# Kernel tuning notes

Hardware: AMD Instinct MI355X
Metric: run time of the kernel (lower is better)

## Reference

```python
import jax, jax.numpy as jnp
import numpy as np

B, T, N = 16, 1024, 128
WIN, STEP = 30, 2
MOMENT_ORDERS = (2, 4, 8)
D_MODEL = 256


def _mask_diag(corr):
    n = corr.shape[-1]
    eye = jnp.eye(n, dtype=corr.dtype)
    return corr * (1.0 - eye) + eye


def corrcoef_time(xw):
    # xw: [..., L, N] -> corr over channels: [..., N, N]
    L = xw.shape[-2]
    xm = xw - xw.mean(axis=-2, keepdims=True)
    cov = jnp.einsum('...ln,...lm->...nm', xm, xm) / (L - 1 + 1e-8)
    var = jnp.clip(jnp.diagonal(cov, axis1=-2, axis2=-1), 1e-8, None)
    std = jnp.sqrt(var)
    corr = cov / (std[..., :, None] * std[..., None, :])
    corr = jnp.nan_to_num(corr, nan=0.0, posinf=0.0, neginf=0.0)
    return _mask_diag(corr)


def rowwise_corr(M):
    # M: [B, N, F]
    Xc = M - M.mean(axis=-1, keepdims=True)
    num = jnp.einsum('bnf,bmf->bnm', Xc, Xc)
    den1 = jnp.sqrt(jnp.clip((Xc ** 2).sum(axis=-1), 1e-8, None))
    corr = num / (den1[:, :, None] * den1[:, None, :])
    corr = jnp.nan_to_num(corr, nan=0.0, posinf=0.0, neginf=0.0)
    return _mask_diag(corr)


def layer_norm(x, gamma, beta, eps=1e-5):
    mu = x.mean(axis=-1, keepdims=True)
    var = ((x - mu) ** 2).mean(axis=-1, keepdims=True)
    return (x - mu) / jnp.sqrt(var + eps) * gamma + beta


def normalize_adj(adj):
    n = adj.shape[-1]
    A_hat = adj + jnp.eye(n, dtype=adj.dtype)
    d = A_hat.sum(axis=-1)
    dis = jnp.sqrt(1.0 / jnp.clip(d, 1e-8, None))
    return A_hat * dis[:, :, None] * dis[:, None, :]


def setup_inputs() -> dict:
    key = jax.random.key(0)
    ks = jax.random.split(key, 8)
    in_dim = len(MOMENT_ORDERS) * N
    return {
        'x': jax.random.normal(ks[0], (B, T, N), dtype=jnp.float32),
        'ln_gamma': jnp.ones((in_dim,), jnp.float32),
        'ln_beta': jnp.zeros((in_dim,), jnp.float32),
        'W1': jax.random.normal(ks[1], (in_dim, D_MODEL), jnp.float32) * 0.05,
        'b1': jnp.zeros((D_MODEL,), jnp.float32),
        'W2': jax.random.normal(ks[2], (D_MODEL, D_MODEL), jnp.float32) * 0.05,
        'b2': jnp.zeros((D_MODEL,), jnp.float32),
        'Wc': jax.random.normal(ks[3], (D_MODEL, 1), jnp.float32) * 0.05,
        'bc': jnp.zeros((1,), jnp.float32),
    }


def reference(x, ln_gamma, ln_beta, W1, b1, W2, b2, Wc, bc):
    # sliding windows (static indices)
    starts = np.arange(0, T - WIN + 1, STEP)
    idx = starts[:, None] + np.arange(WIN)[None, :]
    xw = x[:, idx, :]
    lo = corrcoef_time(xw)                            # [B, Wn, N, N]

    mean_lo = lo.mean(axis=1, keepdims=True)
    centered = lo - mean_lo
    cm_list, ho_list = [], []
    for d in MOMENT_ORDERS:
        cm = jnp.nan_to_num((centered ** d).mean(axis=1),
                            nan=0.0, posinf=0.0, neginf=0.0)  # [B, N, N]
        cm_list.append(cm)
        ho_list.append(rowwise_corr(cm))

    X = jnp.concatenate(cm_list, axis=-1)             # [B, N, 3N]
    X = layer_norm(X, ln_gamma, ln_beta)

    A = jnp.stack(ho_list, axis=1).mean(axis=1)
    A = 0.5 * (A + jnp.swapaxes(A, 1, 2))
    A_norm = normalize_adj(A)

    H = jax.nn.relu(jnp.einsum('bnm,bmd->bnd', A_norm, X @ W1 + b1))
    H = jax.nn.relu(jnp.einsum('bnm,bmd->bnd', A_norm, H @ W2 + b2))
    g = H.mean(axis=1)                                # [B, d_model]
    out = jax.nn.sigmoid(g @ Wc + bc)                 # [B, 1]
    return out
```

## Files before the change

### kernel.cpp

```cpp
#include <hip/hip_runtime.h>
#include <math.h>

#define BB  16
#define TT  1024
#define NN  128
#define WIN 30
#define NWD 498
#define DM  256
#define IND 384
#define GW  16

#define INV_W (1.0f/498.0f)

#define SARR (BB*NN*NN)

#define OFF_A     0
#define OFF_G     (OFF_A    + BB*NWD*NN)
#define OFF_CM2   (OFF_G    + BB*NWD*NN)
#define OFF_CM4   (OFF_CM2  + SARR)
#define OFF_CM8   (OFF_CM4  + SARR)
#define OFF_AD    (OFF_CM8  + SARR)
#define OFF_PART  (OFF_AD   + 3*SARR)
#define OFF_ANORM OFF_PART
#define OFF_BUFA  (OFF_ANORM + SARR)
#define OFF_BUFB  (OFF_BUFA + BB*NN*DM)
#define OFF_CTR   (OFF_PART + 768*16384)
#define OFF_GW1   OFF_A
#define OFF_SG    (OFF_GW1 + IND*DM)
#define OFF_SB    (OFF_SG  + DM)

#define GLL16(gsrc, ldst) \
    __builtin_amdgcn_global_load_lds((const __attribute__((address_space(1))) void*)(gsrc), \
                                     (__attribute__((address_space(3))) void*)(ldst), 16, 0, 0)

__global__ __launch_bounds__(128) void k1_stats(const float* __restrict__ x, float* __restrict__ ws) {
    int bx = blockIdx.x;
    if (bx == 0 && threadIdx.x < 128) ((unsigned*)(ws + OFF_CTR))[threadIdx.x] = 0u;
    int c = bx & 15, b = bx >> 4;
    int w0 = c*32, w1 = min(NWD, w0+32);
    int n = threadIdx.x;
    const float* xp = x + (size_t)b*TT*NN + n;

    float sum = 0.f, sq = 0.f;
    for (int t = 2*w0; t < 2*w0 + WIN; ++t) {
        float v = xp[(size_t)t*NN];
        sum += v; sq = fmaf(v, v, sq);
    }
    for (int w = w0; w < w1; ++w) {
        if (w > w0) {
            float o0 = xp[(size_t)(2*w-2)*NN], o1 = xp[(size_t)(2*w-1)*NN];
            float n0 = xp[(size_t)(2*w+28)*NN], n1 = xp[(size_t)(2*w+29)*NN];
            sum += (n0 + n1) - (o0 + o1);
            sq  += (n0*n0 + n1*n1) - (o0*o0 + o1*o1);
        }
        float mean = sum * (1.0f/30.0f);
        float ss = sq - 30.0f*mean*mean;
        float var = fmaxf(ss * (1.0f/29.0f), 1e-8f);
        float a = (1.0f / sqrtf(var)) * 0.185695338f;
        ws[OFF_A + ((size_t)b*NWD + w)*NN + n] = a;
        ws[OFF_G + ((size_t)b*NWD + w)*NN + n] = mean * a * 5.477225575f;
    }
}

__global__ __launch_bounds__(256) __attribute__((amdgpu_waves_per_eu(3, 3)))
void k24_inc(const float* __restrict__ x, float* __restrict__ ws) {
    __shared__ __align__(16) float xr[64][NN];
    __shared__ __align__(16) float sa[GW][NN];
    __shared__ __align__(16) float sg[GW][NN];
    int bx = blockIdx.x;
    int wc = bx & 7;
    int slab = (bx >> 3) % 6;
    int b = bx / 48;
    const char IS[6] = {0,0,0,0,1,1};
    const char JS[6] = {0,1,2,3,2,3};
    int is = IS[slab], js = JS[slab];
    int w0 = wc * 63, w1 = min(NWD, w0 + 63);
    int tid = threadIdx.x;
    int jg = tid & 7, ig = tid >> 3;
    int i0 = is*64 + ig*2;
    int j0 = js*32 + jg*4;

    const float* xb = x + (size_t)b*TT*NN;
    const float* Ab = ws + OFF_A + (size_t)b*NWD*NN;
    const float* Gb = ws + OFF_G + (size_t)b*NWD*NN;

    float P[2][4];
    float S1[2][4], S2[2][4], S3[2][4], S4[2][4], S5[2][4], S6[2][4], S7[2][4], S8[2][4];
#pragma unroll
    for (int p=0;p<2;++p)
#pragma unroll
        for (int q=0;q<4;++q) {
            P[p][q]=0.f;
            S1[p][q]=0.f;S2[p][q]=0.f;S3[p][q]=0.f;S4[p][q]=0.f;
            S5[p][q]=0.f;S6[p][q]=0.f;S7[p][q]=0.f;S8[p][q]=0.f;
        }

    auto moments = [&](int k) {
        float2 ai = *(const float2*)&sa[k][i0];
        float2 gi = *(const float2*)&sg[k][i0];
        float4 aj = *(const float4*)&sa[k][j0];
        float4 gj = *(const float4*)&sg[k][j0];
        float av[2] = {ai.x, ai.y};
        float mg[2] = {-gi.x, -gi.y};
        float aw[4] = {aj.x, aj.y, aj.z, aj.w};
        float gw[4] = {gj.x, gj.y, gj.z, gj.w};
#pragma unroll
        for (int p=0;p<2;++p)
#pragma unroll
            for (int q=0;q<4;++q) {
                float aa  = av[p]*aw[q];
                float ngg = mg[p]*gw[q];
                float c   = fmaf(P[p][q], aa, ngg);
                float c2 = c*c;
                float c3 = c2*c;
                float c4 = c2*c2;
                S1[p][q] += c;
                S2[p][q] += c2;
                S3[p][q] += c3;
                S4[p][q] += c4;
                S5[p][q] = fmaf(c4, c,  S5[p][q]);
                S6[p][q] = fmaf(c3, c3, S6[p][q]);
                S7[p][q] = fmaf(c3, c4, S7[p][q]);
                S8[p][q] = fmaf(c4, c4, S8[p][q]);
            }
    };

    int rlo = 2*w0;
    for (int wg = w0; wg < w1; wg += GW) {
        int m = min(GW, w1 - wg);
        __syncthreads();
        int rhi = 2*(wg + m - 1) + 29;
        int nr = rhi - rlo + 1;
        for (int idx = tid; idx < nr*32; idx += 256) {
            int r = idx >> 5, c4 = idx & 31;
            int t = rlo + r;
            GLL16(xb + (size_t)t*NN + c4*4, &xr[t & 63][c4*4]);
        }
        for (int idx = tid; idx < m*32; idx += 256) {
            int k = idx >> 5, c4 = idx & 31;
            GLL16(Ab + (size_t)(wg+k)*NN + c4*4, &sa[k][c4*4]);
        }
        for (int idx = tid; idx < m*32; idx += 256) {
            int k = idx >> 5, c4 = idx & 31;
            GLL16(Gb + (size_t)(wg+k)*NN + c4*4, &sg[k][c4*4]);
        }
        rlo = rhi + 1;
        __syncthreads();

        int kstart = 0;
        if (wg == w0) {
#pragma unroll 6
            for (int k = 0; k < WIN; ++k) {
                int t = 2*w0 + k;
                float2 xi = *(const float2*)&xr[t & 63][i0];
                float4 xj = *(const float4*)&xr[t & 63][j0];
                float av[2] = {xi.x, xi.y};
                float bv[4] = {xj.x, xj.y, xj.z, xj.w};
#pragma unroll
                for (int p=0;p<2;++p)
#pragma unroll
                    for (int q=0;q<4;++q) P[p][q] = fmaf(av[p], bv[q], P[p][q]);
            }
            moments(0);
            kstart = 1;
        }
        for (int k = kstart; k < m; ++k) {
            int w = wg + k;
            int tr[4] = {2*w - 2, 2*w - 1, 2*w + 28, 2*w + 29};
#pragma unroll
            for (int kk = 0; kk < 4; ++kk) {
                int t = tr[kk];
                float sgn = (kk < 2) ? -1.0f : 1.0f;
                float2 xi = *(const float2*)&xr[t & 63][i0];
                float4 xj = *(const float4*)&xr[t & 63][j0];
                float av[2] = {sgn*xi.x, sgn*xi.y};
                float bv[4] = {xj.x, xj.y, xj.z, xj.w};
#pragma unroll
                for (int p=0;p<2;++p)
#pragma unroll
                    for (int q=0;q<4;++q) P[p][q] = fmaf(av[p], bv[q], P[p][q]);
            }
            moments(k);
        }
    }

    float* tp = ws + OFF_PART + (size_t)bx*16384 + tid*8;
#define STORE_ARR(A, S) \
    *(float4*)&tp[(A)*2048]     = make_float4(S[0][0], S[0][1], S[0][2], S[0][3]); \
    *(float4*)&tp[(A)*2048 + 4] = make_float4(S[1][0], S[1][1], S[1][2], S[1][3]);
    STORE_ARR(0, S1) STORE_ARR(1, S2) STORE_ARR(2, S3) STORE_ARR(3, S4)
    STORE_ARR(4, S5) STORE_ARR(5, S6) STORE_ARR(6, S7) STORE_ARR(7, S8)
#undef STORE_ARR
}

__global__ __launch_bounds__(256) void kred(const float* __restrict__ gamma, const float* __restrict__ beta,
                                            const float* __restrict__ W1, float* __restrict__ ws) {
    int bxg = blockIdx.x;
    int tid = threadIdx.x;
    if (bxg >= 768) {
        int gi = bxg - 768;
        if (gi < 96) {
#pragma unroll
            for (int kk = 0; kk < 4; ++kk) {
                int k = gi*4 + kk;
                ws[OFF_GW1 + (size_t)k*DM + tid] = gamma[k] * W1[(size_t)k*DM + tid];
            }
        } else {
            float sgv = 0.f, sbv = 0.f;
            for (int k = 0; k < IND; ++k) {
                float w = W1[(size_t)k*DM + tid];
                sgv = fmaf(gamma[k], w, sgv);
                sbv = fmaf(beta[k],  w, sbv);
            }
            ws[OFF_SG + tid] = sgv;
            ws[OFF_SB + tid] = sbv;
        }
        return;
    }
    int pair = bxg >> 3, sub = bxg & 7;
    int b = pair / 6, slab = pair % 6;
    const char IS[6] = {0,0,0,0,1,1};
    const char JS[6] = {0,1,2,3,2,3};
    int is = IS[slab], js = JS[slab];
    int off = sub*256 + tid;
    const float* base = ws + OFF_PART + (size_t)(b*48 + slab*8)*16384;

    float E[8];
#pragma unroll
    for (int a=0;a<8;++a) E[a] = 0.f;
    for (int c = 0; c < 8; ++c) {
        const float* tp = base + (size_t)c*16384;
#pragma unroll
        for (int a=0;a<8;++a) E[a] += tp[a*2048 + off];
    }

    int tid_old = off >> 3, e = off & 7;
    int ig = tid_old >> 3, jg = tid_old & 7;
    int p = e >> 2, q = e & 3;
    int i = is*64 + ig*2 + p;
    int j = js*32 + jg*4 + q;

    float cm2, cm4, cm8;
    if (i == j) {
        cm2 = 0.f; cm4 = 0.f; cm8 = 0.f;
    } else {
        float e1 = E[0]*INV_W, e2 = E[1]*INV_W, e3 = E[2]*INV_W, e4 = E[3]*INV_W;
        float e5 = E[4]*INV_W, e6 = E[5]*INV_W, e7 = E[6]*INV_W, e8 = E[7]*INV_W;
        float m  = e1;
        float m2 = m*m, m3 = m2*m, m4 = m2*m2, m5 = m4*m, m6 = m3*m3, m8 = m4*m4;
        cm2 = e2 - m2;
        cm4 = e4 - 4.f*m*e3 + 6.f*m2*e2 - 3.f*m4;
        cm8 = e8 - 8.f*m*e7 + 28.f*m2*e6 - 56.f*m3*e5 + 70.f*m4*e4
                 - 56.f*m5*e3 + 28.f*m6*e2 - 7.f*m8;
    }
    float* C2 = ws + OFF_CM2 + (size_t)b*NN*NN;
    float* C4 = ws + OFF_CM4 + (size_t)b*NN*NN;
    float* C8 = ws + OFF_CM8 + (size_t)b*NN*NN;
    C2[i*NN + j] = cm2; C2[j*NN + i] = cm2;
    C4[i*NN + j] = cm4; C4[j*NN + i] = cm4;
    C8[i*NN + j] = cm8; C8[j*NN + i] = cm8;
}

#define XSTR 132
__global__ __launch_bounds__(256) void kB(const float* __restrict__ b1, float* __restrict__ ws) {
    __shared__ __align__(16) float smem[64*XSTR + 2*NN];
    __shared__ unsigned winB;
    int blk = blockIdx.x, tid = threadIdx.x;
    if (blk < 192) {
        int rem = blk % 12;
        int b = blk / 12, di = rem >> 2, jq = rem & 3;
        float* Xct = smem;
        float* Mr  = smem + 64*XSTR;
        float* Ir  = Mr + NN;
        const float* cm = ws + (di==0 ? OFF_CM2 : (di==1 ? OFF_CM4 : OFF_CM8)) + (size_t)b*NN*NN;
        int n0 = (tid >> 4)*8, m0 = jq*32 + (tid & 15)*2;
        float s1 = 0.f, s2 = 0.f;
        float acc0[8], acc1[8];
#pragma unroll
        for (int k=0;k<8;++k) { acc0[k]=0.f; acc1[k]=0.f; }

        for (int h = 0; h < 2; ++h) {
            __syncthreads();
            for (int idx = tid; idx < NN*64; idx += 256) {
                int n = idx >> 6, f0 = idx & 63;
                Xct[f0*XSTR + n] = cm[n*NN + h*64 + f0];
            }
            __syncthreads();
            if (tid < NN) {
                for (int f0 = 0; f0 < 64; ++f0) {
                    float v = Xct[f0*XSTR + tid];
                    s1 += v; s2 = fmaf(v, v, s2);
                }
            }
            for (int f0 = 0; f0 < 64; ++f0) {
                const float* row = &Xct[f0*XSTR];
                float4 a0 = *(const float4*)&row[n0];
                float4 a1 = *(const float4*)&row[n0+4];
                float2 bm = *(const float2*)&row[m0];
                float av[8] = {a0.x,a0.y,a0.z,a0.w,a1.x,a1.y,a1.z,a1.w};
#pragma unroll
                for (int k=0;k<8;++k) {
                    acc0[k] = fmaf(av[k], bm.x, acc0[k]);
                    acc1[k] = fmaf(av[k], bm.y, acc1[k]);
                }
            }
        }
        __syncthreads();
        if (tid < NN) {
            float mean = s1 * (1.0f/NN);
            Mr[tid] = mean;
            Ir[tid] = 1.0f/sqrtf(fmaxf(s2 - (float)NN*mean*mean, 1e-8f));
        }
        __syncthreads();
        float rm0 = Mr[m0], rm1 = Mr[m0+1], im0 = Ir[m0], im1 = Ir[m0+1];
        float* Ad = ws + OFF_AD + (size_t)(b*3 + di)*NN*NN;
#pragma unroll
        for (int k=0;k<8;++k) {
            int gi = n0+k;
            float rn = Mr[gi], inv = Ir[gi];
            float v0 = (acc0[k] - (float)NN*rn*rm0) * inv * im0;
            float v1 = (acc1[k] - (float)NN*rn*rm1) * inv * im1;
            if (gi == m0)   v0 = 1.0f;
            if (gi == m0+1) v1 = 1.0f;
            Ad[gi*NN + m0]     = v0;
            Ad[gi*NN + m0 + 1] = v1;
        }

        __syncthreads();
        if (tid == 0) {
            unsigned* ctr = (unsigned*)(ws + OFF_CTR);
            unsigned old = __hip_atomic_fetch_add(&ctr[96 + b], 1u,
                                                  __ATOMIC_ACQ_REL, __HIP_MEMORY_SCOPE_AGENT);
            winB = (old == 11u) ? 1u : 0u;
        }
        __syncthreads();
        if (winB) {
            float* dis = smem;
            const float* A0 = ws + OFF_AD + (size_t)(b*3 + 0)*NN*NN;
            const float* A1 = ws + OFF_AD + (size_t)(b*3 + 1)*NN*NN;
            const float* A2 = ws + OFF_AD + (size_t)(b*3 + 2)*NN*NN;
            if (tid < NN) {
                float d = 1.0f;
                for (int m = 0; m < NN; ++m) {
                    int o = tid*NN + m;
                    d += (A0[o] + A1[o] + A2[o]) * (1.0f/3.0f);
                }
                dis[tid] = sqrtf(1.0f / fmaxf(d, 1e-8f));
            }
            __syncthreads();
            float* An = ws + OFF_ANORM + (size_t)b*NN*NN;
            for (int idx = tid; idx < NN*NN; idx += 256) {
                int n = idx >> 7, m = idx & 127;
                float s = (A0[idx] + A1[idx] + A2[idx]) * (1.0f/3.0f);
                float v = s + (n==m ? 1.0f : 0.0f);
                An[idx] = v * dis[n] * dis[m];
            }
        }
    } else {
        int r0 = (blk - 192) * 4;
        float* sms = smem;
        float* srs = smem + 4;
        {
            int rloc = tid >> 6, lane = tid & 63;
            int grow = r0 + rloc;
            int b = grow >> 7, n = grow & 127;
            const float* c2 = ws + OFF_CM2 + ((size_t)b*NN + n)*NN;
            const float* c4 = ws + OFF_CM4 + ((size_t)b*NN + n)*NN;
            const float* c8 = ws + OFF_CM8 + ((size_t)b*NN + n)*NN;
            float s1 = 0.f, s2 = 0.f;
            for (int e = lane; e < IND; e += 64) {
                float v = (e < 128) ? c2[e] : (e < 256) ? c4[e-128] : c8[e-256];
                s1 += v; s2 = fmaf(v, v, s2);
            }
#pragma unroll
            for (int o = 32; o > 0; o >>= 1) {
                s1 += __shfl_down(s1, o, 64);
                s2 += __shfl_down(s2, o, 64);
            }
            if (lane == 0) {
                float mean = s1 * (1.0f/IND);
                sms[rloc] = mean;
                srs[rloc] = 1.0f / sqrtf(s2*(1.0f/IND) - mean*mean + 1e-5f);
            }
        }
        __syncthreads();
        float mean[4], rstd[4];
        const float* xrow[4];
#pragma unroll
        for (int r = 0; r < 4; ++r) {
            mean[r] = sms[r]; rstd[r] = srs[r];
        }
        float acc[4] = {0.f, 0.f, 0.f, 0.f};
        const float* GW1p = ws + OFF_GW1;
#pragma unroll
        for (int seg = 0; seg < 3; ++seg) {
            int offc = (seg==0) ? OFF_CM2 : (seg==1) ? OFF_CM4 : OFF_CM8;
#pragma unroll
            for (int r = 0; r < 4; ++r) {
                int grow = r0 + r;
                xrow[r] = ws + offc + ((size_t)(grow >> 7)*NN + (grow & 127))*NN;
            }
            const float* gseg = GW1p + (size_t)(seg*128)*DM + tid;
            for (int k = 0; k < 128; k += 2) {
                float g0 = gseg[(size_t)(k+0)*DM];
                float g1 = gseg[(size_t)(k+1)*DM];
#pragma unroll
                for (int r = 0; r < 4; ++r) {
                    acc[r] = fmaf(xrow[r][k+0], g0, acc[r]);
                    acc[r] = fmaf(xrow[r][k+1], g1, acc[r]);
                }
            }
        }
        float sgv = ws[OFF_SG + tid];
        float sbb = ws[OFF_SB + tid] + b1[tid];
        float* O = ws + OFF_BUFA;
#pragma unroll
        for (int r = 0; r < 4; ++r)
            O[(size_t)(r0+r)*DM + tid] = rstd[r]*(acc[r] - mean[r]*sgv) + sbb;
    }
}

__global__ __launch_bounds__(256) void k98_propgemm(const float* __restrict__ W2, const float* __restrict__ b2,
                                                    const float* __restrict__ An, const float* __restrict__ Zin,
                                                    float* __restrict__ Out) {
    __shared__ float Hs[8][DM];
    int bx = blockIdx.x;
    int b = bx >> 4, n0 = (bx & 15)*8;
    int tid = threadIdx.x;
    const float* A = An + (size_t)b*NN*NN + (size_t)n0*NN;
    const float* Z = Zin + (size_t)b*NN*DM;
    float acc[8] = {0,0,0,0,0,0,0,0};
    for (int m = 0; m < NN; m += 4) {
        float z0 = Z[(size_t)(m+0)*DM + tid];
        float z1 = Z[(size_t)(m+1)*DM + tid];
        float z2 = Z[(size_t)(m+2)*DM + tid];
        float z3 = Z[(size_t)(m+3)*DM + tid];
#pragma unroll
        for (int r = 0; r < 8; ++r) {
            const float* Ar = A + r*NN + m;
            acc[r] = fmaf(Ar[0], z0, acc[r]);
            acc[r] = fmaf(Ar[1], z1, acc[r]);
            acc[r] = fmaf(Ar[2], z2, acc[r]);
            acc[r] = fmaf(Ar[3], z3, acc[r]);
        }
    }
#pragma unroll
    for (int r = 0; r < 8; ++r) Hs[r][tid] = fmaxf(acc[r], 0.0f);
    __syncthreads();
    float acc2[8];
    float bv = b2[tid];
#pragma unroll
    for (int r = 0; r < 8; ++r) acc2[r] = bv;
    for (int k = 0; k < DM; k += 4) {
        float w0 = W2[(size_t)(k+0)*DM + tid];
        float w1 = W2[(size_t)(k+1)*DM + tid];
        float w2 = W2[(size_t)(k+2)*DM + tid];
        float w3 = W2[(size_t)(k+3)*DM + tid];
#pragma unroll
        for (int r = 0; r < 8; ++r) {
            float4 h = *(const float4*)&Hs[r][k];
            acc2[r] = fmaf(h.x, w0, acc2[r]);
            acc2[r] = fmaf(h.y, w1, acc2[r]);
            acc2[r] = fmaf(h.z, w2, acc2[r]);
            acc2[r] = fmaf(h.w, w3, acc2[r]);
        }
    }
    float* O = Out + (size_t)b*NN*DM;
#pragma unroll
    for (int r = 0; r < 8; ++r) O[(size_t)(n0+r)*DM + tid] = acc2[r];
}

__global__ __launch_bounds__(256) void k9_prop(const float* __restrict__ Wc, const float* __restrict__ bc,
                                               const float* __restrict__ An, const float* __restrict__ Zin,
                                               float* __restrict__ Out,
                                               float* __restrict__ ws, float* __restrict__ outp) {
    __shared__ float red[256];
    __shared__ unsigned win9;
    int bx = blockIdx.x;
    int b = bx >> 4, n0 = (bx & 15)*8;
    int tid = threadIdx.x;
    const float* A = An + (size_t)b*NN*NN + (size_t)n0*NN;
    const float* Z = Zin + (size_t)b*NN*DM;
    float acc[8] = {0,0,0,0,0,0,0,0};
    for (int m = 0; m < NN; m += 4) {
        float z0 = Z[(size_t)(m+0)*DM + tid];
        float z1 = Z[(size_t)(m+1)*DM + tid];
        float z2 = Z[(size_t)(m+2)*DM + tid];
        float z3 = Z[(size_t)(m+3)*DM + tid];
#pragma unroll
        for (int r = 0; r < 8; ++r) {
            const float* Ar = A + r*NN + m;
            acc[r] = fmaf(Ar[0], z0, acc[r]);
            acc[r] = fmaf(Ar[1], z1, acc[r]);
            acc[r] = fmaf(Ar[2], z2, acc[r]);
            acc[r] = fmaf(Ar[3], z3, acc[r]);
        }
    }
    float* O = Out + (size_t)b*NN*DM;
#pragma unroll
    for (int r = 0; r < 8; ++r) O[(size_t)(n0+r)*DM + tid] = fmaxf(acc[r], 0.0f);

    __syncthreads();
    if (tid == 0) {
        unsigned* ctr = (unsigned*)(ws + OFF_CTR);
        unsigned old = __hip_atomic_fetch_add(&ctr[112 + b], 1u,
                                              __ATOMIC_ACQ_REL, __HIP_MEMORY_SCOPE_AGENT);
        win9 = (old == 15u) ? 1u : 0u;
    }
    __syncthreads();
    if (win9) {
        const float* H = Out + (size_t)b*NN*DM;
        float s = 0.f;
        for (int n = 0; n < NN; ++n) s += H[(size_t)n*DM + tid];
        red[tid] = s * (1.0f/NN) * Wc[tid];
        __syncthreads();
        for (int o = 128; o > 0; o >>= 1) { if (tid < o) red[tid] += red[tid+o]; __syncthreads(); }
        if (tid == 0) outp[b] = 1.0f/(1.0f + expf(-(red[0] + bc[0])));
    }
}

extern "C" void kernel_launch(void* const* d_in, const int* in_sizes, int n_in,
                              void* d_out, int out_size, void* d_ws, size_t ws_size,
                              hipStream_t stream) {
    (void)in_sizes; (void)n_in; (void)out_size; (void)ws_size;
    const float* x     = (const float*)d_in[0];
    const float* gamma = (const float*)d_in[1];
    const float* beta  = (const float*)d_in[2];
    const float* W1    = (const float*)d_in[3];
    const float* b1    = (const float*)d_in[4];
    const float* W2    = (const float*)d_in[5];
    const float* b2    = (const float*)d_in[6];
    const float* Wc    = (const float*)d_in[7];
    const float* bc    = (const float*)d_in[8];
    float* ws  = (float*)d_ws;
    float* out = (float*)d_out;

    k1_stats    <<<BB*16,    128, 0, stream>>>(x, ws);
    k24_inc     <<<BB*6*8,   256, 0, stream>>>(x, ws);
    kred        <<<768+96+1, 256, 0, stream>>>(gamma, beta, W1, ws);
    kB          <<<704,      256, 0, stream>>>(b1, ws);
    k98_propgemm<<<BB*16,    256, 0, stream>>>(W2, b2, ws + OFF_ANORM, ws + OFF_BUFA, ws + OFF_BUFB);
    k9_prop     <<<BB*16,    256, 0, stream>>>(Wc, bc, ws + OFF_ANORM, ws + OFF_BUFB, ws + OFF_BUFA, ws, out);
}
```

Baseline: 233.5 us.

## Double k24_inc threads with 2x2 per-thread tiles and XCD-aware block mapping

```diff
diff --git a/kernel.cpp b/kernel.cpp
--- a/kernel.cpp
+++ b/kernel.cpp
@@ -62,34 +62,35 @@
     }
 }
 
-__global__ __launch_bounds__(256) __attribute__((amdgpu_waves_per_eu(3, 3)))
+__global__ __launch_bounds__(512) __attribute__((amdgpu_waves_per_eu(6, 6)))
 void k24_inc(const float* __restrict__ x, float* __restrict__ ws) {
     __shared__ __align__(16) float xr[64][NN];
     __shared__ __align__(16) float sa[GW][NN];
     __shared__ __align__(16) float sg[GW][NN];
-    int bx = blockIdx.x;
-    int wc = bx & 7;
-    int slab = (bx >> 3) % 6;
-    int b = bx / 48;
+    int pbx = blockIdx.x;
+    int xcd = pbx & 7, rest = pbx >> 3;
+    int wc = rest & 7, pg = rest >> 3;
+    int pair = pg*8 + xcd;
+    int b = pair / 6, slab = pair % 6;
     const char IS[6] = {0,0,0,0,1,1};
     const char JS[6] = {0,1,2,3,2,3};
     int is = IS[slab], js = JS[slab];
     int w0 = wc * 63, w1 = min(NWD, w0 + 63);
     int tid = threadIdx.x;
-    int jg = tid & 7, ig = tid >> 3;
+    int jg = tid & 15, ig = tid >> 4;
     int i0 = is*64 + ig*2;
-    int j0 = js*32 + jg*4;
+    int j0 = js*32 + jg*2;
 
     const float* xb = x + (size_t)b*TT*NN;
     const float* Ab = ws + OFF_A + (size_t)b*NWD*NN;
     const float* Gb = ws + OFF_G + (size_t)b*NWD*NN;
 
-    float P[2][4];
-    float S1[2][4], S2[2][4], S3[2][4], S4[2][4], S5[2][4], S6[2][4], S7[2][4], S8[2][4];
+    float P[2][2];
+    float S1[2][2], S2[2][2], S3[2][2], S4[2][2], S5[2][2], S6[2][2], S7[2][2], S8[2][2];
 #pragma unroll
     for (int p=0;p<2;++p)
 #pragma unroll
-        for (int q=0;q<4;++q) {
+        for (int q=0;q<2;++q) {
             P[p][q]=0.f;
             S1[p][q]=0.f;S2[p][q]=0.f;S3[p][q]=0.f;S4[p][q]=0.f;
             S5[p][q]=0.f;S6[p][q]=0.f;S7[p][q]=0.f;S8[p][q]=0.f;
@@ -98,16 +99,16 @@
     auto moments = [&](int k) {
         float2 ai = *(const float2*)&sa[k][i0];
         float2 gi = *(const float2*)&sg[k][i0];
-        float4 aj = *(const float4*)&sa[k][j0];
-        float4 gj = *(const float4*)&sg[k][j0];
+        float2 aj = *(const float2*)&sa[k][j0];
+        float2 gj = *(const float2*)&sg[k][j0];
         float av[2] = {ai.x, ai.y};
         float mg[2] = {-gi.x, -gi.y};
-        float aw[4] = {aj.x, aj.y, aj.z, aj.w};
-        float gw[4] = {gj.x, gj.y, gj.z, gj.w};
+        float aw[2] = {aj.x, aj.y};
+        float gw[2] = {gj.x, gj.y};
 #pragma unroll
         for (int p=0;p<2;++p)
 #pragma unroll
-            for (int q=0;q<4;++q) {
+            for (int q=0;q<2;++q) {
                 float aa  = av[p]*aw[q];
                 float ngg = mg[p]*gw[q];
                 float c   = fmaf(P[p][q], aa, ngg);
@@ -131,16 +132,16 @@
         __syncthreads();
         int rhi = 2*(wg + m - 1) + 29;
         int nr = rhi - rlo + 1;
-        for (int idx = tid; idx < nr*32; idx += 256) {
+        for (int idx = tid; idx < nr*32; idx += 512) {
             int r = idx >> 5, c4 = idx & 31;
             int t = rlo + r;
             GLL16(xb + (size_t)t*NN + c4*4, &xr[t & 63][c4*4]);
         }
-        for (int idx = tid; idx < m*32; idx += 256) {
+        for (int idx = tid; idx < m*32; idx += 512) {
             int k = idx >> 5, c4 = idx & 31;
             GLL16(Ab + (size_t)(wg+k)*NN + c4*4, &sa[k][c4*4]);
         }
-        for (int idx = tid; idx < m*32; idx += 256) {
+        for (int idx = tid; idx < m*32; idx += 512) {
             int k = idx >> 5, c4 = idx & 31;
             GLL16(Gb + (size_t)(wg+k)*NN + c4*4, &sg[k][c4*4]);
         }
@@ -153,13 +154,13 @@
             for (int k = 0; k < WIN; ++k) {
                 int t = 2*w0 + k;
                 float2 xi = *(const float2*)&xr[t & 63][i0];
-                float4 xj = *(const float4*)&xr[t & 63][j0];
+                float2 xj = *(const float2*)&xr[t & 63][j0];
                 float av[2] = {xi.x, xi.y};
-                float bv[4] = {xj.x, xj.y, xj.z, xj.w};
+                float bv[2] = {xj.x, xj.y};
 #pragma unroll
                 for (int p=0;p<2;++p)
 #pragma unroll
-                    for (int q=0;q<4;++q) P[p][q] = fmaf(av[p], bv[q], P[p][q]);
+                    for (int q=0;q<2;++q) P[p][q] = fmaf(av[p], bv[q], P[p][q]);
             }
             moments(0);
             kstart = 1;
@@ -172,22 +173,21 @@
                 int t = tr[kk];
                 float sgn = (kk < 2) ? -1.0f : 1.0f;
                 float2 xi = *(const float2*)&xr[t & 63][i0];
-                float4 xj = *(const float4*)&xr[t & 63][j0];
+                float2 xj = *(const float2*)&xr[t & 63][j0];
                 float av[2] = {sgn*xi.x, sgn*xi.y};
-                float bv[4] = {xj.x, xj.y, xj.z, xj.w};
+                float bv[2] = {xj.x, xj.y};
 #pragma unroll
                 for (int p=0;p<2;++p)
 #pragma unroll
-                    for (int q=0;q<4;++q) P[p][q] = fmaf(av[p], bv[q], P[p][q]);
+                    for (int q=0;q<2;++q) P[p][q] = fmaf(av[p], bv[q], P[p][q]);
             }
             moments(k);
         }
     }
 
-    float* tp = ws + OFF_PART + (size_t)bx*16384 + tid*8;
+    float* tp = ws + OFF_PART + (size_t)(b*48 + slab*8 + wc)*16384 + tid*4;
 #define STORE_ARR(A, S) \
-    *(float4*)&tp[(A)*2048]     = make_float4(S[0][0], S[0][1], S[0][2], S[0][3]); \
-    *(float4*)&tp[(A)*2048 + 4] = make_float4(S[1][0], S[1][1], S[1][2], S[1][3]);
+    *(float4*)&tp[(A)*2048] = make_float4(S[0][0], S[0][1], S[1][0], S[1][1]);
     STORE_ARR(0, S1) STORE_ARR(1, S2) STORE_ARR(2, S3) STORE_ARR(3, S4)
     STORE_ARR(4, S5) STORE_ARR(5, S6) STORE_ARR(6, S7) STORE_ARR(7, S8)
 #undef STORE_ARR
@@ -217,7 +217,9 @@
         }
         return;
     }
-    int pair = bxg >> 3, sub = bxg & 7;
+    int xcd = bxg & 7, rest = bxg >> 3;
+    int sub = rest & 7, pg = rest >> 3;
+    int pair = pg*8 + xcd;
     int b = pair / 6, slab = pair % 6;
     const char IS[6] = {0,0,0,0,1,1};
     const char JS[6] = {0,1,2,3,2,3};
@@ -234,11 +236,11 @@
         for (int a=0;a<8;++a) E[a] += tp[a*2048 + off];
     }
 
-    int tid_old = off >> 3, e = off & 7;
-    int ig = tid_old >> 3, jg = tid_old & 7;
-    int p = e >> 2, q = e & 3;
+    int tid_old = off >> 2, e = off & 3;
+    int ig = tid_old >> 4, jg = tid_old & 15;
+    int p = e >> 1, q = e & 1;
     int i = is*64 + ig*2 + p;
-    int j = js*32 + jg*4 + q;
+    int j = js*32 + jg*2 + q;
 
     float cm2, cm4, cm8;
     if (i == j) {
@@ -536,7 +538,7 @@
     float* out = (float*)d_out;
 
     k1_stats    <<<BB*16,    128, 0, stream>>>(x, ws);
-    k24_inc     <<<BB*6*8,   256, 0, stream>>>(x, ws);
+    k24_inc     <<<BB*6*8,   512, 0, stream>>>(x, ws);
     kred        <<<768+96+1, 256, 0, stream>>>(gamma, beta, W1, ws);
     kB          <<<704,      256, 0, stream>>>(b1, ws);
     k98_propgemm<<<BB*16,    256, 0, stream>>>(W2, b2, ws + OFF_ANORM, ws + OFF_BUFA, ws + OFF_BUFB);
```

Result: slower. 242.1 us (+3.7%).
